# Kernel optimization log

Measured on AMD Instinct MI355X. Metric: run time of the kernel, lower is better.

The kernel has to match this reference:

```python
import jax, jax.numpy as jnp
import numpy as np
from jax import lax

H = 12  # num_heads (from init_kwargs)


def _orthogonal_landmarks(q, num_landmarks):
    # q: (B, N, D) already scaled. Faithful to torch loop: recursively pick the
    # point whose max |cos sim| to the already-selected landmarks is minimal.
    B, N, D = q.shape
    nrm = jnp.linalg.norm(q, axis=-1, keepdims=True)
    qk = q / jnp.maximum(nrm, 1e-12)
    bidx = jnp.arange(B)
    key = jax.random.key(42)
    idx0 = jax.random.randint(key, (B,), 0, N)
    cur = qk[bidx, idx0]                             # (B, D)
    # running max |cos sim|; selected rows pinned to 10 (as in torch code)
    max_sim = jnp.zeros((B, N), qk.dtype).at[bidx, idx0].set(10.0)

    def step(carry, _):
        max_sim, cur = carry
        cos = jnp.abs(jnp.einsum('bnd,bd->bn', qk, cur))
        max_sim = jnp.maximum(max_sim, cos)
        idx = jnp.argmin(max_sim, axis=-1)
        cur2 = qk[bidx, idx]
        max_sim = max_sim.at[bidx, idx].set(10.0)
        return (max_sim, cur2), idx

    (_, _), idxs = lax.scan(step, (max_sim, cur), None, length=num_landmarks - 1)
    all_idx = jnp.concatenate([idx0[None, :], idxs], axis=0).T  # (B, L)
    landmarks = q[bidx[:, None], all_idx]                        # unnormalized q rows
    return lax.stop_gradient(landmarks)


def _orthoformer(q, k, v, num_landmarks, num_frames):
    # q,k,v: (B*h, N, D);  N = F * P
    Bh, N, D = q.shape
    F = num_frames
    P = N // F
    sc = D ** (-0.25)
    q = q * sc
    k = k * sc
    lm = _orthogonal_landmarks(q, num_landmarks)                 # (Bh, L, D)
    kernel_1 = jax.nn.softmax(jnp.einsum('bnd,bld->bnl', q, lm), axis=-1)   # (Bh,N,L)
    k2 = jnp.einsum('bld,bnd->bln', lm, k).reshape(Bh, num_landmarks, F, P)
    kernel_2 = jax.nn.softmax(k2, axis=-1)                       # (Bh,L,F,P)
    vr = v.reshape(Bh, F, P, D)
    x = jnp.einsum('blfp,bfpd->blfd', kernel_2, vr)
    x = jnp.einsum('bnl,blfd->bnfd', kernel_1, x)                # (Bh,N,F,D)
    return x


def setup_inputs() -> dict:
    key = jax.random.key(0)
    ks = jax.random.split(key, 6)
    B, F, P, C = 2, 16, 196, 768
    N = F * P
    s = 0.02
    x = jax.random.normal(ks[0], (B, N, C), jnp.float32)
    W_qkv = jax.random.normal(ks[1], (C, 3 * C), jnp.float32) * s
    W_pq = jax.random.normal(ks[2], (C, C), jnp.float32) * s
    W_pkv = jax.random.normal(ks[3], (C, 2 * C), jnp.float32) * s
    W_proj = jax.random.normal(ks[4], (C, C), jnp.float32) * s
    b_proj = jnp.zeros((C,), jnp.float32)
    return {"x": x, "W_qkv": W_qkv, "W_pq": W_pq, "W_pkv": W_pkv,
            "W_proj": W_proj, "b_proj": b_proj,
            "seq_len": P, "num_frames": F, "num_landmarks": 128}


def reference(x, W_qkv, W_pq, W_pkv, W_proj, b_proj, seq_len, num_frames, num_landmarks):
    B, N, C = x.shape
    F, P, h = num_frames, seq_len, H
    d = C // h
    scale = d ** (-0.5)
    qkv = x @ W_qkv                                              # (B,N,3C)
    q, k, v = jnp.split(qkv, 3, axis=-1)
    def to_bh(t):  # b n (h d) -> (b h) n d
        return t.reshape(B, N, h, d).transpose(0, 2, 1, 3).reshape(B * h, N, d)
    q_, k_, v_ = to_bh(q), to_bh(k), to_bh(v)
    xo = _orthoformer(q_, k_, v_, num_landmarks, F)              # (B*h,N,F,d)
    # (b h) s f d -> b s f (h d)
    xo = xo.reshape(B, h, N, F, d).transpose(0, 2, 3, 1, 4).reshape(B, N, F, C)
    # diagonal over (frame-of-query g, frame-of-key f)
    xd = xo.reshape(B, F, P, F, C)
    xdiag = jnp.diagonal(xd, axis1=1, axis2=3)                   # (B,P,C,F)
    xdiag = jnp.moveaxis(xdiag, -1, 1).reshape(B, N, C)          # b (f p) d
    q2 = xdiag @ W_pq                                            # (B,N,C)
    k2, v2 = jnp.split(xo @ W_pkv, 2, axis=-1)                   # (B,N,F,C) each
    q2 = q2.reshape(B, N, h, d).transpose(0, 2, 1, 3) * scale    # (B,h,N,d)
    k2 = k2.reshape(B, N, F, h, d).transpose(0, 3, 1, 2, 4)      # (B,h,N,F,d)
    v2 = v2.reshape(B, N, F, h, d).transpose(0, 3, 1, 2, 4)
    attn = jax.nn.softmax(jnp.einsum('bhsd,bhsfd->bhsf', q2, k2), axis=-1)
    out = jnp.einsum('bhsf,bhsfd->bhsd', attn, v2)               # (B,h,N,d)
    out = out.transpose(0, 2, 1, 3).reshape(B, N, C)
    out = out @ W_proj + b_proj
    return out, attn
```

## Files before the change

kernel.cpp:

```cpp
#include <hip/hip_runtime.h>


using u16 = unsigned short;
using u32 = unsigned int;
using u64 = unsigned long long;

typedef short bf16x8 __attribute__((ext_vector_type(8)));
typedef float f32x4 __attribute__((ext_vector_type(4)));

#define N_ 3136
#define C_ 768
#define H_ 12
#define F_ 16
#define P_ 196
#define L_ 128
#define SC_ 0.35355339059327373f
#define OUTPART_ ((size_t)2 * N_ * C_)
#define KB_ 8
#define RPB_ 392

__device__ __forceinline__ float b2f(u16 u) {
  u32 x = ((u32)u) << 16; float f; __builtin_memcpy(&f, &x, 4); return f;
}
__device__ __forceinline__ float lo16f(u32 u) {
  u32 x = u << 16; float f; __builtin_memcpy(&f, &x, 4); return f;
}
__device__ __forceinline__ float hi16f(u32 u) {
  u32 x = u & 0xFFFF0000u; float f; __builtin_memcpy(&f, &x, 4); return f;
}
__device__ __forceinline__ u16 f2b(float f) {
  u32 u; __builtin_memcpy(&u, &f, 4);
  u32 r = (u + 0x7FFFu + ((u >> 16) & 1u)) >> 16;
  return (u16)r;
}
__device__ __forceinline__ u64 d2u(double d) { u64 u; __builtin_memcpy(&u, &d, 8); return u; }

__device__ __forceinline__ void gll16(const void* g, void* l) {
  __builtin_amdgcn_global_load_lds(
      (__attribute__((address_space(1))) void*)g,
      (__attribute__((address_space(3))) void*)l, 16, 0, 0);
}

__global__ void detect_k(const u32* __restrict__ w, int* __restrict__ flag) {
  const int t = threadIdx.x;
  int hits = 0;
  #pragma unroll
  for (int i = 0; i < 16; ++i) {
    u32 word = w[t * 16 + i];
    u32 e = (word >> 7) & 0xFFu;
    if (e >= 110u && e <= 126u) hits++;
  }
  #pragma unroll
  for (int off = 32; off > 0; off >>= 1) hits += __shfl_down(hits, off);
  if (t == 0) flag[0] = (hits >= 512) ? 0 : 1;
}

__global__ void zcnt_k(u64* __restrict__ p) { if (threadIdx.x < 384) p[threadIdx.x] = 0ull; }

__device__ __forceinline__ void tf2(u32 k0, u32 k1v, u32 c0, u32 c1, u32& o0, u32& o1) {
  u32 ks[3] = {k0, k1v, k0 ^ k1v ^ 0x1BD11BDAu};
  u32 x0 = c0 + ks[0], x1 = c1 + ks[1];
  const u32 rA[4] = {13u, 15u, 26u, 6u}, rB[4] = {17u, 29u, 16u, 24u};
  #pragma unroll
  for (int r = 0; r < 5; ++r) {
    #pragma unroll
    for (int q = 0; q < 4; ++q) {
      u32 rot = (r & 1) ? rB[q] : rA[q];
      x0 += x1; x1 = (x1 << rot) | (x1 >> (32u - rot)); x1 ^= x0;
    }
    x0 += ks[(r + 1) % 3];
    x1 += ks[(r + 2) % 3] + (u32)(r + 1);
  }
  o0 = x0; o1 = x1;
}

__device__ __forceinline__ int tf_idx0(int bh) {
  u32 a0, a1, b0, b1;
  tf2(0u, 42u, 0u, 0u, a0, a1);
  tf2(0u, 42u, 0u, 1u, b0, b1);
  u32 j = (u32)bh;
  u32 h0, h1, l0, l1;
  tf2(a0, a1, 0u, j, h0, h1);
  u32 hi = h0 ^ h1;
  tf2(b0, b1, 0u, j, l0, l1);
  u32 lo = l0 ^ l1;
  return (int)(((hi % 3136u) * 2048u + (lo % 3136u)) % 3136u);
}

__global__ __launch_bounds__(256) void qselT_k(const void* __restrict__ xr, const void* __restrict__ wr,
                                               const int* __restrict__ flagp, float* __restrict__ qt)
{
  __shared__ float As[128 * 20];
  __shared__ float Bs[16 * 64];
  const int t = threadIdx.x;
  const int m0 = blockIdx.x * 128;
  const int n0 = blockIdx.y * 64;
  const int f32i = flagp[0];
  const int tx = t & 15, ty = t >> 4;
  float acc[8][4];
  #pragma unroll
  for (int i = 0; i < 8; ++i)
    #pragma unroll
    for (int j = 0; j < 4; ++j) acc[i][j] = 0.f;

  const int alr = t >> 1;
  const int alk = (t & 1) * 8;
  const int bkr = t >> 4;
  const int bnc = (t & 15) * 4;

  for (int k0 = 0; k0 < 768; k0 += 16) {
    float av[8];
    float4 bv;
    if (f32i) {
      const float* xa = (const float*)xr + (size_t)(m0 + alr) * 768 + k0 + alk;
      float4 a0 = *(const float4*)(xa);
      float4 a1 = *(const float4*)(xa + 4);
      av[0] = a0.x; av[1] = a0.y; av[2] = a0.z; av[3] = a0.w;
      av[4] = a1.x; av[5] = a1.y; av[6] = a1.z; av[7] = a1.w;
      bv = *(const float4*)((const float*)wr + (size_t)(k0 + bkr) * 2304 + n0 + bnc);
    } else {
      const u16* xa = (const u16*)xr + (size_t)(m0 + alr) * 768 + k0 + alk;
      #pragma unroll
      for (int j = 0; j < 8; ++j) av[j] = b2f(xa[j]);
      const u16* wa = (const u16*)wr + (size_t)(k0 + bkr) * 2304 + n0 + bnc;
      bv.x = b2f(wa[0]); bv.y = b2f(wa[1]); bv.z = b2f(wa[2]); bv.w = b2f(wa[3]);
    }
    #pragma unroll
    for (int j = 0; j < 8; ++j) As[alr * 20 + alk + j] = av[j];
    *(float4*)(&Bs[bkr * 64 + bnc]) = bv;
    __syncthreads();
    #pragma unroll
    for (int kk = 0; kk < 16; ++kk) {
      float a[8], b[4];
      #pragma unroll
      for (int i = 0; i < 8; ++i) a[i] = As[(ty * 8 + i) * 20 + kk];
      #pragma unroll
      for (int j = 0; j < 4; ++j) b[j] = Bs[kk * 64 + tx * 4 + j];
      #pragma unroll
      for (int i = 0; i < 8; ++i)
        #pragma unroll
        for (int j = 0; j < 4; ++j) acc[i][j] += a[i] * b[j];
    }
    __syncthreads();
  }
  #pragma unroll
  for (int i = 0; i < 8; ++i) {
    const int m = m0 + ty * 8 + i;
    const int b = m / N_, n = m - b * N_;
    #pragma unroll
    for (int j = 0; j < 4; ++j) {
      const int col = n0 + tx * 4 + j;
      const int hh = col >> 6, dd = col & 63;
      qt[((size_t)(b * H_ + hh) * 64 + dd) * N_ + n] = acc[i][j] * SC_;
    }
  }
}

__global__ __launch_bounds__(512, 1) void landmarksR_k(
    const float* __restrict__ qt, float* __restrict__ lm, u64* __restrict__ cand)
{
  const int kb = blockIdx.y;
  const int bh = blockIdx.x;
  const float* QT = qt + (size_t)bh * 64 * N_;
  float* LM = lm + (size_t)bh * L_ * 64;
  u64* cd = cand + (size_t)bh * 16;
  __shared__ double curD[64];
  __shared__ u64 redV[8];
  __shared__ int redI[8];
  __shared__ int sW;
  const int t = threadIdx.x;
  const bool act = (t < RPB_);
  const int g = t >> 2, dc = t & 3, d0 = dc * 16;
  const int r0 = kb * RPB_;
  const int myRow = r0 + t;
  const float* base = QT + r0 + 4 * g;

  float4 qreg[16];
  #pragma unroll
  for (int i = 0; i < 16; ++i) qreg[i] = (float4){0.f, 0.f, 0.f, 0.f};
  if (act) {
    #pragma unroll
    for (int i = 0; i < 16; ++i) qreg[i] = *(const float4*)(base + (size_t)(d0 + i) * N_);
  }

  double inv_own = 0.0, ms_own = 0.0;
  if (act) {
    double s0 = 0.0, s1 = 0.0, s2 = 0.0, s3 = 0.0;
    #pragma unroll
    for (int i = 0; i < 16; ++i) {
      const float4 v = qreg[i];
      s0 += (double)v.x * (double)v.x; s1 += (double)v.y * (double)v.y;
      s2 += (double)v.z * (double)v.z; s3 += (double)v.w * (double)v.w;
    }
    s0 += __shfl_xor(s0, 1); s1 += __shfl_xor(s1, 1);
    s2 += __shfl_xor(s2, 1); s3 += __shfl_xor(s3, 1);
    s0 += __shfl_xor(s0, 2); s1 += __shfl_xor(s1, 2);
    s2 += __shfl_xor(s2, 2); s3 += __shfl_xor(s3, 2);
    const double sown = (dc == 0) ? s0 : (dc == 1) ? s1 : (dc == 2) ? s2 : s3;
    inv_own = 1.0 / fmax(sqrt(sown), 1e-12);
  }
  const int idx0 = tf_idx0(bh);
  if (act && myRow == idx0) ms_own = 10.0;

  if (t < 64) {
    const float vf = QT[(size_t)t * N_ + idx0];
    double v = (double)vf;
    double s = v * v;
    #pragma unroll
    for (int off = 32; off; off >>= 1) s += __shfl_xor(s, off);
    curD[t] = v / fmax(sqrt(s), 1e-12);
    if (kb == 0) LM[t] = vf;
  }
  __syncthreads();

  for (int step = 1; step < 128; ++step) {
    u64 bV = d2u(1e30); int bI = 0x7fffffff;
    if (act) {
      double a0 = 0.0, a1 = 0.0, a2 = 0.0, a3 = 0.0;
      #pragma unroll
      for (int i = 0; i < 16; ++i) {
        const float4 v = qreg[i];
        const double c = curD[d0 + i];
        a0 += (double)v.x * c; a1 += (double)v.y * c;
        a2 += (double)v.z * c; a3 += (double)v.w * c;
      }
      a0 += __shfl_xor(a0, 1); a1 += __shfl_xor(a1, 1);
      a2 += __shfl_xor(a2, 1); a3 += __shfl_xor(a3, 1);
      a0 += __shfl_xor(a0, 2); a1 += __shfl_xor(a1, 2);
      a2 += __shfl_xor(a2, 2); a3 += __shfl_xor(a3, 2);
      const double aown = (dc == 0) ? a0 : (dc == 1) ? a1 : (dc == 2) ? a2 : a3;
      ms_own = fmax(ms_own, fabs(aown * inv_own));
      bV = d2u(ms_own); bI = myRow;
    }
    #pragma unroll
    for (int off = 32; off; off >>= 1) {
      const u64 ov = __shfl_xor(bV, off);
      const int oi = __shfl_xor(bI, off);
      if (ov < bV || (ov == bV && oi < bI)) { bV = ov; bI = oi; }
    }
    if ((t & 63) == 0) { redV[t >> 6] = bV; redI[t >> 6] = bI; }
    __syncthreads();
    const int par = step & 1;
    if (t == 0) {
      u64 v = redV[0]; int ix = redI[0];
      #pragma unroll
      for (int w2 = 1; w2 < 8; ++w2)
        if (redV[w2] < v || (redV[w2] == v && redI[w2] < ix)) { v = redV[w2]; ix = redI[w2]; }
      const u64 pk = (v & ~((1ull << 19) - 1ull)) | ((u64)(u32)(step & 127) << 12) | (u64)(u32)ix;
      __hip_atomic_store(&cd[par * KB_ + kb], pk, __ATOMIC_RELAXED, __HIP_MEMORY_SCOPE_AGENT);
    }
    if (t < 64) {
      u64 pv = ~0ull;
      int ok = 1;
      for (;;) {
        if (t < KB_) {
          pv = __hip_atomic_load(&cd[par * KB_ + t], __ATOMIC_RELAXED, __HIP_MEMORY_SCOPE_AGENT);
          ok = ((int)((pv >> 12) & 127u) == step) ? 1 : 0;
        }
        if (__all(ok)) break;
        __builtin_amdgcn_s_sleep(1);
      }
      u64 m = (t < KB_) ? pv : ~0ull;
      #pragma unroll
      for (int off = 1; off < KB_; off <<= 1) {
        const u64 o = __shfl_xor(m, off);
        if (o < m) m = o;
      }
      if (t == 0) sW = (int)(m & 0xFFFu);
    }
    __syncthreads();
    const int w = sW;
    if (act && myRow == w) ms_own = 10.0;
    if (t < 64) {
      const float vf = QT[(size_t)t * N_ + w];
      double v = (double)vf;
      double s = v * v;
      #pragma unroll
      for (int off = 32; off; off >>= 1) s += __shfl_xor(s, off);
      curD[t] = v / fmax(sqrt(s), 1e-12);
      if (kb == 0) LM[(size_t)step * 64 + t] = vf;
    }
    __syncthreads();
  }
}

__device__ __forceinline__ void twT_body(const void* W, int K, int Nn, int f32i,
                                         u16* WT, int k0, int n0, int t, u16 (&Ts)[64][80])
{
  const int kr = t >> 2, nc = (t & 3) * 16;
  u16 tmp[16];
  if (f32i) {
    const float* p = (const float*)W + (size_t)(k0 + kr) * Nn + n0 + nc;
    #pragma unroll
    for (int j = 0; j < 16; ++j) tmp[j] = f2b(p[j]);
  } else {
    const u16* p = (const u16*)W + (size_t)(k0 + kr) * Nn + n0 + nc;
    #pragma unroll
    for (int j = 0; j < 16; ++j) tmp[j] = p[j];
  }
  #pragma unroll
  for (int j = 0; j < 16; ++j) Ts[kr][nc + j] = tmp[j];
  __syncthreads();
  const int nr = t >> 2, kc = (t & 3) * 16;
  u16 o[16];
  #pragma unroll
  for (int j = 0; j < 16; ++j) o[j] = Ts[kc + j][nr];
  u16* dst = WT + (size_t)(n0 + nr) * K + k0 + kc;
  *(uint4*)(dst) = *(uint4*)(o);
  *(uint4*)(dst + 8) = *(uint4*)(o + 8);
}

__global__ __launch_bounds__(256) void twT_k(const void* __restrict__ W, int K, int Nn,
                                             const int* __restrict__ flagp, u16* __restrict__ WT)
{
  __shared__ u16 Ts[64][80];
  twT_body(W, K, Nn, flagp[0], WT, blockIdx.x * 64, blockIdx.y * 64, threadIdx.x, Ts);
}

__global__ __launch_bounds__(256) void twT3_k(const void* __restrict__ W0, const void* __restrict__ W1,
                                              const void* __restrict__ W2, const int* __restrict__ flagp,
                                              u16* __restrict__ T0, u16* __restrict__ T1, u16* __restrict__ T2,
                                              u16* __restrict__ Wb)
{
  __shared__ u16 Ts[64][80];
  const int z = blockIdx.z;
  const int t = threadIdx.x;
  if (z == 3) {
    const int k0 = blockIdx.x * 64, n0 = blockIdx.y * 64;
    const int kr = t >> 2, nc = (t & 3) * 16;
    u16 tmp[16];
    if (flagp[0]) {
      const float* p = (const float*)W0 + (size_t)(k0 + kr) * 1536 + n0 + nc;
      #pragma unroll
      for (int j = 0; j < 16; ++j) tmp[j] = f2b(p[j]);
    } else {
      const u16* p = (const u16*)W0 + (size_t)(k0 + kr) * 1536 + n0 + nc;
      #pragma unroll
      for (int j = 0; j < 16; ++j) tmp[j] = p[j];
    }
    u16* dst = Wb + (size_t)(k0 + kr) * 1536 + n0 + nc;
    *(uint4*)(dst) = *(uint4*)(tmp);
    *(uint4*)(dst + 8) = *(uint4*)(tmp + 8);
    return;
  }
  const void* W = (z == 0) ? W0 : (z == 1) ? W1 : W2;
  u16* WT = (z == 0) ? T0 : (z == 1) ? T1 : T2;
  const int Nn = (z == 0) ? 1536 : 768;
  if (blockIdx.y * 64 >= Nn) return;
  twT_body(W, 768, Nn, flagp[0], WT, blockIdx.x * 64, blockIdx.y * 64, t, Ts);
}

__global__ __launch_bounds__(256) void xcvt_k(const void* __restrict__ x,
                                              const int* __restrict__ flagp, u16* __restrict__ xb)
{
  const int i = blockIdx.x * 256 + threadIdx.x;
  if (flagp[0]) {
    const float4* p = (const float4*)x + (size_t)i * 2;
    float4 f0 = p[0], f1 = p[1];
    u16 tmp[8] = { f2b(f0.x), f2b(f0.y), f2b(f0.z), f2b(f0.w),
                   f2b(f1.x), f2b(f1.y), f2b(f1.z), f2b(f1.w) };
    *(uint4*)(xb + (size_t)i * 8) = *(uint4*)tmp;
  } else {
    ((uint4*)xb)[i] = ((const uint4*)x)[i];
  }
}

struct GemmCore {
  const u16 *aP0, *aP1, *bP0, *bP1;
  u16 *lA0, *lA1, *lB0, *lB1;
  int roA[4], roB[4];
  int mw, nw, lr, lk;
};

__device__ __forceinline__ void gemm_core_init(GemmCore& gc, u16* As, u16* Bs,
    const u16* A16, const u16* B16, size_t aOff, size_t bOff,
    int m0, int n0, int lda, int ldb, int M, int t)
{
  const int lane = t & 63;
  const int w = t >> 6;
  gc.mw = (w >> 1) * 64;
  gc.nw = (w & 1) * 64;
  gc.lr = lane & 15;
  gc.lk = lane >> 4;
  const int c0 = w * 2, c1 = c0 + 1;
  const int rl = lane >> 2, sl = lane & 3;
  const int rowA0 = c0 * 16 + rl, rowA1 = c1 * 16 + rl;
  const int segA0 = (sl ^ ((rowA0 ^ (rowA0 >> 2)) & 3)) * 8;
  const int segA1 = (sl ^ ((rowA1 ^ (rowA1 >> 2)) & 3)) * 8;
  int ga0 = m0 + rowA0; if (ga0 >= M) ga0 = M - 1;
  int ga1 = m0 + rowA1; if (ga1 >= M) ga1 = M - 1;
  gc.aP0 = A16 + aOff + (size_t)ga0 * lda + segA0;
  gc.aP1 = A16 + aOff + (size_t)ga1 * lda + segA1;
  gc.bP0 = B16 + bOff + (size_t)(n0 + rowA0) * ldb + segA0;
  gc.bP1 = B16 + bOff + (size_t)(n0 + rowA1) * ldb + segA1;
  gc.lA0 = &As[c0 * 512]; gc.lA1 = &As[c1 * 512];
  gc.lB0 = &Bs[c0 * 512]; gc.lB1 = &Bs[c1 * 512];
  #pragma unroll
  for (int q = 0; q < 4; ++q) {
    const int ra = gc.mw + q * 16 + gc.lr;
    gc.roA[q] = ra * 32 + ((gc.lk ^ ((ra ^ (ra >> 2)) & 3)) * 8);
    const int rb = gc.nw + q * 16 + gc.lr;
    gc.roB[q] = rb * 32 + ((gc.lk ^ ((rb ^ (rb >> 2)) & 3)) * 8);
  }
}

__device__ __forceinline__ void gemm_core_loop(const GemmCore& gc, u16* As, u16* Bs,
                                               int K, f32x4 (&acc)[4][4])
{
  for (int k0 = 0; k0 < K; k0 += 32) {
    gll16(gc.aP0 + k0, gc.lA0);
    gll16(gc.aP1 + k0, gc.lA1);
    gll16(gc.bP0 + k0, gc.lB0);
    gll16(gc.bP1 + k0, gc.lB1);
    __syncthreads();
    bf16x8 af[4], bfv[4];
    #pragma unroll
    for (int mt = 0; mt < 4; ++mt) af[mt] = *(const bf16x8*)(&As[gc.roA[mt]]);
    #pragma unroll
    for (int nt = 0; nt < 4; ++nt) bfv[nt] = *(const bf16x8*)(&Bs[gc.roB[nt]]);
    #pragma unroll
    for (int mt = 0; mt < 4; ++mt)
      #pragma unroll
      for (int nt = 0; nt < 4; ++nt)
        acc[mt][nt] = __builtin_amdgcn_mfma_f32_16x16x32_bf16(af[mt], bfv[nt], acc[mt][nt], 0, 0, 0);
    __syncthreads();
  }
}

template <int MODE>
__global__ __launch_bounds__(256) void gemm_k(
    const void* __restrict__ Ap, const void* __restrict__ Bp,
    int M, int K, int lda, int ldb, int n0c, int cn, const int* __restrict__ flagp,
    float* __restrict__ of0, u16* __restrict__ ob0, u16* __restrict__ ob1, u16* __restrict__ ob2,
    const void* __restrict__ biasRaw, void* __restrict__ outRaw)
{
  __shared__ u16 As[128 * 32];
  __shared__ u16 Bs[128 * 32];
  const int t = threadIdx.x;
  const int m0 = blockIdx.x * 128;
  const int n0 = blockIdx.y * 128;
  const int rf = (MODE == 4) ? flagp[0] : 0;

  size_t aOff = 0, bOff = 0;
  if constexpr (MODE == 1) {
    const int bh = blockIdx.z;
    aOff = (size_t)bh * ((size_t)N_ * 128) + (size_t)n0c * 128;
    bOff = (size_t)bh * (1024 * 128);
  }
  if constexpr (MODE == 5) {
    const int h = blockIdx.z;
    aOff = (size_t)h * (2 * cn) * 64;
    bOff = (size_t)h * 64;
  }
  if constexpr (MODE == 6) {
    const int h = blockIdx.z;
    aOff = (size_t)h * (2 * cn) * 768;
    bOff = (size_t)(768 + h * 64) * 768;
  }
  f32x4 acc[4][4];
  #pragma unroll
  for (int i = 0; i < 4; ++i)
    #pragma unroll
    for (int j = 0; j < 4; ++j) acc[i][j] = (f32x4){0.f, 0.f, 0.f, 0.f};

  GemmCore gc;
  gemm_core_init(gc, As, Bs, (const u16*)Ap, (const u16*)Bp, aOff, bOff, m0, n0, lda, ldb, M, t);
  gemm_core_loop(gc, As, Bs, K, acc);

  const int lr = gc.lr, lk = gc.lk, mw = gc.mw, nw = gc.nw;
  #pragma unroll
  for (int mt = 0; mt < 4; ++mt) {
    #pragma unroll
    for (int nt = 0; nt < 4; ++nt) {
      #pragma unroll
      for (int r = 0; r < 4; ++r) {
        const int grow = m0 + mw + mt * 16 + lk * 4 + r;
        const int gcol = n0 + nw + nt * 16 + lr;
        if (grow >= M) continue;
        float vv = acc[mt][nt][r];
        if constexpr (MODE == 0) {
          int b = (grow >= N_) ? 1 : 0;
          int n = grow - b * N_;
          int t3 = gcol / C_, cc = gcol - t3 * C_;
          int hh = cc >> 6, dd = cc & 63;
          size_t dst = (((size_t)(b * H_ + hh)) * N_ + n) * 64 + dd;
          if (t3 == 0) ob0[dst] = f2b(vv * SC_);
          else if (t3 == 1) ob1[dst] = f2b(vv * SC_);
          else ob2[dst] = f2b(vv);
        } else if constexpr (MODE == 1) {
          const int bh = blockIdx.z;
          int b = bh / H_, hh = bh - b * H_;
          int f = gcol >> 6, dd = gcol & 63;
          u16 wv = f2b(vv);
          ob0[(((size_t)(b * cn + grow)) * F_ + f) * C_ + hh * 64 + dd] = wv;
          int n = n0c + grow;
          if (f == n / P_) ob1[((size_t)(b * cn + grow)) * C_ + hh * 64 + dd] = wv;
        } else if constexpr (MODE == 3) {
          int hh = gcol >> 6, dd = gcol & 63;
          ob0[((size_t)hh * (2 * cn) + grow) * 64 + dd] = f2b(vv * 0.125f);
        } else if constexpr (MODE == 5) {
          ob0[((size_t)blockIdx.z * (2 * cn) + grow) * 768 + gcol] = f2b(vv);
        } else if constexpr (MODE == 6) {
          if (gcol < 64) {
            int b2 = (grow >= cn) ? 1 : 0;
            int ln = grow - b2 * cn;
            ob0[((size_t)(b2 * N_ + n0c + ln)) * 768 + blockIdx.z * 64 + gcol] = f2b(vv);
          }
        } else {
          float bvad = rf ? ((const float*)biasRaw)[gcol] : b2f(((const u16*)biasRaw)[gcol]);
          float ov = vv + bvad;
          if (rf) ((float*)outRaw)[(size_t)grow * C_ + gcol] = ov;
          else    ((u16*)outRaw)[(size_t)grow * C_ + gcol] = f2b(ov);
        }
      }
    }
  }
}

__global__ __launch_bounds__(256) void k1_k(const u16* __restrict__ qb,
                                            const float* __restrict__ lm,
                                            u16* __restrict__ k1)
{
  const int bh = blockIdx.y;
  const int r0 = blockIdx.x * 64;
  __shared__ float qT[64][65];
  __shared__ float lmS[128 * 64];
  __shared__ float redA[4][64];
  __shared__ float redB[64];
  const int t = threadIdx.x;
  const u16* Q = qb + ((size_t)bh * N_ + r0) * 64;
  const float* Lm = lm + (size_t)bh * L_ * 64;
  for (int u = t; u < 2048; u += 256) ((float4*)lmS)[u] = ((const float4*)Lm)[u];
  for (int u = t; u < 512; u += 256) {
    int row = u >> 3, j0 = (u & 7) * 8;
    uint4 pk = *(const uint4*)(Q + (size_t)row * 64 + j0);
    const u16* pu = (const u16*)&pk;
    #pragma unroll
    for (int jj = 0; jj < 8; ++jj) qT[j0 + jj][row] = b2f(pu[jj]);
  }
  __syncthreads();
  const int row = t & 63, ch = t >> 6;
  float qr[64];
  #pragma unroll
  for (int j = 0; j < 64; ++j) qr[j] = qT[j][row];
  float s[32];
  for (int li = 0; li < 32; ++li) {
    const float* lp = lmS + (ch * 32 + li) * 64;
    float a = 0.f;
    #pragma unroll
    for (int j = 0; j < 64; ++j) a += lp[j] * qr[j];
    s[li] = a;
  }
  float mx = -1e30f;
  for (int li = 0; li < 32; ++li) mx = fmaxf(mx, s[li]);
  redA[ch][row] = mx;
  __syncthreads();
  if (t < 64) redB[t] = fmaxf(fmaxf(redA[0][t], redA[1][t]), fmaxf(redA[2][t], redA[3][t]));
  __syncthreads();
  mx = redB[row];
  float sum = 0.f;
  for (int li = 0; li < 32; ++li) { float e = __expf(s[li] - mx); s[li] = e; sum += e; }
  __syncthreads();
  redA[ch][row] = sum;
  __syncthreads();
  if (t < 64) redB[t] = 1.0f / (redA[0][t] + redA[1][t] + redA[2][t] + redA[3][t]);
  __syncthreads();
  const float inv = redB[row];
  u16* out = k1 + ((size_t)bh * N_ + r0 + row) * 128 + ch * 32;
  for (int li = 0; li < 32; ++li) out[li] = f2b(s[li] * inv);
}

__global__ __launch_bounds__(256) void k2x1_k(const float* __restrict__ lm,
                                              const u16* __restrict__ kb,
                                              const u16* __restrict__ vb,
                                              u16* __restrict__ x1)
{
  const int bh = blockIdx.x;
  const int f = blockIdx.y;
  __shared__ u16 kS[P_ * 64];
  __shared__ u16 vS[P_ * 64];
  __shared__ float redM[2][128];
  __shared__ float redS[2][128];
  const int t = threadIdx.x;
  const u16* Kf = kb + ((size_t)bh * N_ + f * P_) * 64;
  const u16* Vf = vb + ((size_t)bh * N_ + f * P_) * 64;
  for (int u = t; u < 1568; u += 256) {
    ((uint4*)kS)[u] = ((const uint4*)Kf)[u];
    ((uint4*)vS)[u] = ((const uint4*)Vf)[u];
  }
  __syncthreads();
  const int l = t & 127, half = t >> 7;
  const float* lp = lm + ((size_t)bh * L_ + l) * 64;
  float lr[64];
  #pragma unroll
  for (int j = 0; j < 64; ++j) lr[j] = lp[j];

  const int p0 = half * 98, p1 = p0 + 98;
  float mx = -1e30f;
  for (int p = p0; p < p1; ++p) {
    const uint4* kp = (const uint4*)(kS + p * 64);
    float s = 0.f;
    #pragma unroll
    for (int q4 = 0; q4 < 8; ++q4) {
      uint4 pk = kp[q4];
      const u32* pu = (const u32*)&pk;
      #pragma unroll
      for (int j2 = 0; j2 < 4; ++j2) {
        u32 u = pu[j2];
        s += lr[q4 * 8 + j2 * 2] * lo16f(u) + lr[q4 * 8 + j2 * 2 + 1] * hi16f(u);
      }
    }
    mx = fmaxf(mx, s);
  }
  redM[half][l] = mx;
  __syncthreads();
  mx = fmaxf(redM[0][l], redM[1][l]);

  float sm = 0.f;
  for (int p = p0; p < p1; ++p) {
    const uint4* kp = (const uint4*)(kS + p * 64);
    float s = 0.f;
    #pragma unroll
    for (int q4 = 0; q4 < 8; ++q4) {
      uint4 pk = kp[q4];
      const u32* pu = (const u32*)&pk;
      #pragma unroll
      for (int j2 = 0; j2 < 4; ++j2) {
        u32 u = pu[j2];
        s += lr[q4 * 8 + j2 * 2] * lo16f(u) + lr[q4 * 8 + j2 * 2 + 1] * hi16f(u);
      }
    }
    sm += __expf(s - mx);
  }
  redS[half][l] = sm;
  __syncthreads();
  const float inv = 1.0f / (redS[0][l] + redS[1][l]);

  const int dd0 = half * 32;
  float acc[32];
  #pragma unroll
  for (int u = 0; u < 32; ++u) acc[u] = 0.f;
  for (int p = 0; p < P_; ++p) {
    const uint4* kp = (const uint4*)(kS + p * 64);
    float s = 0.f;
    #pragma unroll
    for (int q4 = 0; q4 < 8; ++q4) {
      uint4 pk = kp[q4];
      const u32* pu = (const u32*)&pk;
      #pragma unroll
      for (int j2 = 0; j2 < 4; ++j2) {
        u32 u = pu[j2];
        s += lr[q4 * 8 + j2 * 2] * lo16f(u) + lr[q4 * 8 + j2 * 2 + 1] * hi16f(u);
      }
    }
    const float e = __expf(s - mx);
    const uint4* vp = (const uint4*)(vS + p * 64 + dd0);
    #pragma unroll
    for (int q4 = 0; q4 < 4; ++q4) {
      uint4 pv = vp[q4];
      const u32* pu = (const u32*)&pv;
      #pragma unroll
      for (int j2 = 0; j2 < 4; ++j2) {
        u32 u = pu[j2];
        acc[q4 * 8 + j2 * 2]     += e * lo16f(u);
        acc[q4 * 8 + j2 * 2 + 1] += e * hi16f(u);
      }
    }
  }
  u16* outT = x1 + (size_t)bh * (1024 * 128) + (size_t)(f * 64 + dd0) * 128 + l;
  for (int u = 0; u < 32; ++u) outT[(size_t)u * 128] = f2b(acc[u] * inv);
}

__global__ __launch_bounds__(256) void attn2_k(const u16* __restrict__ xoc,
                                               const u16* __restrict__ g,
                                               int n0c, int cn, const int* __restrict__ flagp,
                                               void* __restrict__ outRaw, u16* __restrict__ wc)
{
  __shared__ float aS[12][16];
  const int t = threadIdx.x;
  const int m = blockIdx.x;
  const int b = (m >= cn) ? 1 : 0;
  const int ln = m - b * cn;
  const int n = n0c + ln;
  const int f32o = flagp[0];
  const u16* Xo = xoc + ((size_t)(b * cn + ln) * 16) * 768;
  const size_t hstr = (size_t)(2 * cn) * 768;

  if (t < 192) {
    const int h = t >> 4, f = t & 15;
    const uint4* xp = (const uint4*)(Xo + (size_t)f * 768);
    const uint4* gp = (const uint4*)(g + (size_t)h * hstr + (size_t)m * 768);
    float lg = 0.f;
    #pragma unroll 4
    for (int q = 0; q < 96; ++q) {
      uint4 xv = xp[q], gv = gp[q];
      const u32* xu = (const u32*)&xv;
      const u32* gu = (const u32*)&gv;
      #pragma unroll
      for (int j = 0; j < 4; ++j)
        lg += lo16f(xu[j]) * lo16f(gu[j]) + hi16f(xu[j]) * hi16f(gu[j]);
    }
    float mx = lg;
    mx = fmaxf(mx, __shfl_xor(mx, 1));
    mx = fmaxf(mx, __shfl_xor(mx, 2));
    mx = fmaxf(mx, __shfl_xor(mx, 4));
    mx = fmaxf(mx, __shfl_xor(mx, 8));
    float e = __expf(lg - mx);
    float sm = e;
    sm += __shfl_xor(sm, 1);
    sm += __shfl_xor(sm, 2);
    sm += __shfl_xor(sm, 4);
    sm += __shfl_xor(sm, 8);
    const float a = e / sm;
    const size_t abase = ((size_t)(b * H_ + h) * N_ + n) * F_ + f;
    if (f32o) ((float*)outRaw)[OUTPART_ + abase] = a;
    else      ((u16*)outRaw)[OUTPART_ + abase] = f2b(a);
    aS[h][f] = a;
  }
  __syncthreads();
  if (t < 192) {
    const int cg = t >> 1, sh = t & 1;
    const int c0 = cg * 8;
    float acc[6][8];
    #pragma unroll
    for (int j = 0; j < 6; ++j)
      #pragma unroll
      for (int k = 0; k < 8; ++k) acc[j][k] = 0.f;
    for (int f = 0; f < 16; ++f) {
      uint4 xv = *(const uint4*)(Xo + (size_t)f * 768 + c0);
      const u32* xu = (const u32*)&xv;
      float xf[8];
      #pragma unroll
      for (int j = 0; j < 4; ++j) { xf[2 * j] = lo16f(xu[j]); xf[2 * j + 1] = hi16f(xu[j]); }
      #pragma unroll
      for (int j = 0; j < 6; ++j) {
        const float a = aS[sh * 6 + j][f];
        #pragma unroll
        for (int k = 0; k < 8; ++k) acc[j][k] += a * xf[k];
      }
    }
    #pragma unroll
    for (int j = 0; j < 6; ++j) {
      u16 pk[8];
      #pragma unroll
      for (int k = 0; k < 8; ++k) pk[k] = f2b(acc[j][k]);
      *(uint4*)(wc + (size_t)(sh * 6 + j) * hstr + (size_t)m * 768 + c0) = *(uint4*)pk;
    }
  }
}

extern "C" void kernel_launch(void* const* d_in, const int* in_sizes, int n_in,
                              void* d_out, int out_size, void* d_ws, size_t ws_size,
                              hipStream_t stream)
{
  (void)in_sizes; (void)n_in; (void)out_size;
  const void* x     = d_in[0];
  const void* Wqkv  = d_in[1];
  const void* Wpq   = d_in[2];
  const void* Wpkv  = d_in[3];
  const void* Wproj = d_in[4];
  const void* bproj = d_in[5];

  char* ws = (char*)d_ws;
  size_t off = 0;
  auto alloc = [&](size_t bytes) { void* p = ws + off; off += (bytes + 255) & ~(size_t)255; return p; };
  int*  flagp  = (int*)alloc(256);
  u16*  WpkvT  = (u16*)alloc(2359296);
  u16*  WpqT   = (u16*)alloc(1179648);
  u16*  WprojT = (u16*)alloc(1179648);
  u16*  Wpkvb  = (u16*)alloc(2359296);
  float* lm    = (float*)alloc(786432);
  u16*  x1b    = (u16*)alloc(6291456);
  u16*  ob     = (u16*)alloc(9633792);
  u16*  k1b    = (u16*)alloc(19267584);
  const size_t sc0 = off;

  float* qt   = (float*)(ws + sc0);
  u64*   cand = (u64*)(ws + sc0 + 19267584);
  u16* WqkvT = (u16*)(ws + sc0);
  u16* xb    = (u16*)(ws + sc0 + 3538944);
  u16* qb    = (u16*)(ws + sc0 + 13172736);
  u16* kbuf  = qb + 4816896;
  u16* vb    = kbuf + 4816896;
  const size_t phaseB_need = sc0 + 42074112 + 1024;
  if (phaseB_need > ws_size) return;

  int Nc = 0;
  {
    const int cands[5] = {3136, 1568, 784, 392, 196};
    for (int i = 0; i < 5; ++i) {
      if (sc0 + (size_t)92160 * cands[i] + 1024 <= ws_size) { Nc = cands[i]; break; }
    }
  }
  if (Nc == 0) return;
  const int nchunks = N_ / Nc;
  u16* xoc = (u16*)(ws + sc0);
  u16* xdc = xoc + (size_t)24576 * Nc;
  u16* q2b = xdc + (size_t)1536 * Nc;
  u16* gbf = q2b + (size_t)1536 * Nc;

  detect_k<<<1, 64, 0, stream>>>((const u32*)Wqkv, flagp);
  zcnt_k<<<1, 512, 0, stream>>>(cand);
  twT3_k<<<dim3(12, 24, 4), 256, 0, stream>>>(Wpkv, Wpq, Wproj, flagp,
                                              WpkvT, WpqT, WprojT, Wpkvb);

  qselT_k<<<dim3(49, 12), 256, 0, stream>>>(x, Wqkv, flagp, qt);
  landmarksR_k<<<dim3(24, KB_), 512, 0, stream>>>(qt, lm, cand);

  twT_k<<<dim3(12, 36), 256, 0, stream>>>(Wqkv, 768, 2304, flagp, WqkvT);
  xcvt_k<<<2352, 256, 0, stream>>>(x, flagp, xb);

  gemm_k<0><<<dim3(49, 18, 1), 256, 0, stream>>>(xb, WqkvT, 6272, 768, 768, 768, 0, 0, flagp,
                                                 nullptr, qb, kbuf, vb, nullptr, nullptr);
  k2x1_k<<<dim3(24, 16), 256, 0, stream>>>(lm, kbuf, vb, x1b);
  k1_k<<<dim3(49, 24), 256, 0, stream>>>(qb, lm, k1b);

  const int gx = (2 * Nc + 127) / 128;
  for (int c = 0; c < nchunks; ++c) {
    const int n0c = c * Nc;
    gemm_k<1><<<dim3((Nc + 127) / 128, 8, 24), 256, 0, stream>>>(
        k1b, x1b, Nc, 128, 128, 128, n0c, Nc, flagp, nullptr, xoc, xdc, nullptr, nullptr, nullptr);
    gemm_k<3><<<dim3(gx, 6, 1), 256, 0, stream>>>(
        xdc, WpqT, 2 * Nc, 768, 768, 768, n0c, Nc, flagp, nullptr, q2b, nullptr, nullptr, nullptr, nullptr);
    gemm_k<5><<<dim3(gx, 6, 12), 256, 0, stream>>>(
        q2b, Wpkvb, 2 * Nc, 64, 64, 1536, n0c, Nc, flagp, nullptr, gbf, nullptr, nullptr, nullptr, nullptr);
    attn2_k<<<dim3(2 * Nc), 256, 0, stream>>>(xoc, gbf, n0c, Nc, flagp, d_out, gbf);
    gemm_k<6><<<dim3(gx, 1, 12), 256, 0, stream>>>(
        gbf, WpkvT, 2 * Nc, 768, 768, 768, n0c, Nc, flagp, nullptr, ob, nullptr, nullptr, nullptr, nullptr);
  }
  gemm_k<4><<<dim3(49, 6, 1), 256, 0, stream>>>(ob, WprojT, 6272, 768, 768, 768, 0, 0, flagp,
                                                nullptr, nullptr, nullptr, nullptr, bproj, d_out);
}
```

Baseline: 1.522 ms.

## Overlap serial landmark selection with QKV GEMM in fused kernels

Merges the q-projection, WqkvT transpose and x conversion into one launch, then runs the serial landmark-selection blocks and the QKV GEMM blocks in a single launch so the GEMM fills CUs left idle by the latency-bound landmark loop. This requires a new workspace layout with separate regions so qt, xb/WqkvT and qb/k/v do not alias, and keeps a fallback path when the workspace is too small. The risk is that landmark blocks, which spin across blocks, could be starved if they are not all resident, and the 512-thread GEMM blocks leave half their threads idle.

```diff
diff --git a/kernel.cpp b/kernel.cpp
--- a/kernel.cpp
+++ b/kernel.cpp
@@ -87,15 +87,10 @@
   return (int)(((hi % 3136u) * 2048u + (lo % 3136u)) % 3136u);
 }
 
-__global__ __launch_bounds__(256) void qselT_k(const void* __restrict__ xr, const void* __restrict__ wr,
-                                               const int* __restrict__ flagp, float* __restrict__ qt)
-{
-  __shared__ float As[128 * 20];
-  __shared__ float Bs[16 * 64];
-  const int t = threadIdx.x;
-  const int m0 = blockIdx.x * 128;
-  const int n0 = blockIdx.y * 64;
-  const int f32i = flagp[0];
+__device__ __forceinline__ void qsel_body(const void* xr, const void* wr, int f32i,
+                                          float* qt, int m0, int n0, int t,
+                                          float* As, float* Bs)
+{
   const int tx = t & 15, ty = t >> 4;
   float acc[8][4];
   #pragma unroll
@@ -156,132 +151,12 @@
   }
 }
 
-__global__ __launch_bounds__(512, 1) void landmarksR_k(
-    const float* __restrict__ qt, float* __restrict__ lm, u64* __restrict__ cand)
-{
-  const int kb = blockIdx.y;
-  const int bh = blockIdx.x;
-  const float* QT = qt + (size_t)bh * 64 * N_;
-  float* LM = lm + (size_t)bh * L_ * 64;
-  u64* cd = cand + (size_t)bh * 16;
-  __shared__ double curD[64];
-  __shared__ u64 redV[8];
-  __shared__ int redI[8];
-  __shared__ int sW;
-  const int t = threadIdx.x;
-  const bool act = (t < RPB_);
-  const int g = t >> 2, dc = t & 3, d0 = dc * 16;
-  const int r0 = kb * RPB_;
-  const int myRow = r0 + t;
-  const float* base = QT + r0 + 4 * g;
-
-  float4 qreg[16];
-  #pragma unroll
-  for (int i = 0; i < 16; ++i) qreg[i] = (float4){0.f, 0.f, 0.f, 0.f};
-  if (act) {
-    #pragma unroll
-    for (int i = 0; i < 16; ++i) qreg[i] = *(const float4*)(base + (size_t)(d0 + i) * N_);
-  }
-
-  double inv_own = 0.0, ms_own = 0.0;
-  if (act) {
-    double s0 = 0.0, s1 = 0.0, s2 = 0.0, s3 = 0.0;
-    #pragma unroll
-    for (int i = 0; i < 16; ++i) {
-      const float4 v = qreg[i];
-      s0 += (double)v.x * (double)v.x; s1 += (double)v.y * (double)v.y;
-      s2 += (double)v.z * (double)v.z; s3 += (double)v.w * (double)v.w;
-    }
-    s0 += __shfl_xor(s0, 1); s1 += __shfl_xor(s1, 1);
-    s2 += __shfl_xor(s2, 1); s3 += __shfl_xor(s3, 1);
-    s0 += __shfl_xor(s0, 2); s1 += __shfl_xor(s1, 2);
-    s2 += __shfl_xor(s2, 2); s3 += __shfl_xor(s3, 2);
-    const double sown = (dc == 0) ? s0 : (dc == 1) ? s1 : (dc == 2) ? s2 : s3;
-    inv_own = 1.0 / fmax(sqrt(sown), 1e-12);
-  }
-  const int idx0 = tf_idx0(bh);
-  if (act && myRow == idx0) ms_own = 10.0;
-
-  if (t < 64) {
-    const float vf = QT[(size_t)t * N_ + idx0];
-    double v = (double)vf;
-    double s = v * v;
-    #pragma unroll
-    for (int off = 32; off; off >>= 1) s += __shfl_xor(s, off);
-    curD[t] = v / fmax(sqrt(s), 1e-12);
-    if (kb == 0) LM[t] = vf;
-  }
-  __syncthreads();
-
-  for (int step = 1; step < 128; ++step) {
-    u64 bV = d2u(1e30); int bI = 0x7fffffff;
-    if (act) {
-      double a0 = 0.0, a1 = 0.0, a2 = 0.0, a3 = 0.0;
-      #pragma unroll
-      for (int i = 0; i < 16; ++i) {
-        const float4 v = qreg[i];
-        const double c = curD[d0 + i];
-        a0 += (double)v.x * c; a1 += (double)v.y * c;
-        a2 += (double)v.z * c; a3 += (double)v.w * c;
-      }
-      a0 += __shfl_xor(a0, 1); a1 += __shfl_xor(a1, 1);
-      a2 += __shfl_xor(a2, 1); a3 += __shfl_xor(a3, 1);
-      a0 += __shfl_xor(a0, 2); a1 += __shfl_xor(a1, 2);
-      a2 += __shfl_xor(a2, 2); a3 += __shfl_xor(a3, 2);
-      const double aown = (dc == 0) ? a0 : (dc == 1) ? a1 : (dc == 2) ? a2 : a3;
-      ms_own = fmax(ms_own, fabs(aown * inv_own));
-      bV = d2u(ms_own); bI = myRow;
-    }
-    #pragma unroll
-    for (int off = 32; off; off >>= 1) {
-      const u64 ov = __shfl_xor(bV, off);
-      const int oi = __shfl_xor(bI, off);
-      if (ov < bV || (ov == bV && oi < bI)) { bV = ov; bI = oi; }
-    }
-    if ((t & 63) == 0) { redV[t >> 6] = bV; redI[t >> 6] = bI; }
-    __syncthreads();
-    const int par = step & 1;
-    if (t == 0) {
-      u64 v = redV[0]; int ix = redI[0];
-      #pragma unroll
-      for (int w2 = 1; w2 < 8; ++w2)
-        if (redV[w2] < v || (redV[w2] == v && redI[w2] < ix)) { v = redV[w2]; ix = redI[w2]; }
-      const u64 pk = (v & ~((1ull << 19) - 1ull)) | ((u64)(u32)(step & 127) << 12) | (u64)(u32)ix;
-      __hip_atomic_store(&cd[par * KB_ + kb], pk, __ATOMIC_RELAXED, __HIP_MEMORY_SCOPE_AGENT);
-    }
-    if (t < 64) {
-      u64 pv = ~0ull;
-      int ok = 1;
-      for (;;) {
-        if (t < KB_) {
-          pv = __hip_atomic_load(&cd[par * KB_ + t], __ATOMIC_RELAXED, __HIP_MEMORY_SCOPE_AGENT);
-          ok = ((int)((pv >> 12) & 127u) == step) ? 1 : 0;
-        }
-        if (__all(ok)) break;
-        __builtin_amdgcn_s_sleep(1);
-      }
-      u64 m = (t < KB_) ? pv : ~0ull;
-      #pragma unroll
-      for (int off = 1; off < KB_; off <<= 1) {
-        const u64 o = __shfl_xor(m, off);
-        if (o < m) m = o;
-      }
-      if (t == 0) sW = (int)(m & 0xFFFu);
-    }
-    __syncthreads();
-    const int w = sW;
-    if (act && myRow == w) ms_own = 10.0;
-    if (t < 64) {
-      const float vf = QT[(size_t)t * N_ + w];
-      double v = (double)vf;
-      double s = v * v;
-      #pragma unroll
-      for (int off = 32; off; off >>= 1) s += __shfl_xor(s, off);
-      curD[t] = v / fmax(sqrt(s), 1e-12);
-      if (kb == 0) LM[(size_t)step * 64 + t] = vf;
-    }
-    __syncthreads();
-  }
+__global__ __launch_bounds__(256) void qselT_k(const void* __restrict__ xr, const void* __restrict__ wr,
+                                               const int* __restrict__ flagp, float* __restrict__ qt)
+{
+  __shared__ float As[128 * 20];
+  __shared__ float Bs[16 * 64];
+  qsel_body(xr, wr, flagp[0], qt, blockIdx.x * 128, blockIdx.y * 64, threadIdx.x, As, Bs);
 }
 
 __device__ __forceinline__ void twT_body(const void* W, int K, int Nn, int f32i,
@@ -350,11 +225,9 @@
   twT_body(W, 768, Nn, flagp[0], WT, blockIdx.x * 64, blockIdx.y * 64, t, Ts);
 }
 
-__global__ __launch_bounds__(256) void xcvt_k(const void* __restrict__ x,
-                                              const int* __restrict__ flagp, u16* __restrict__ xb)
-{
-  const int i = blockIdx.x * 256 + threadIdx.x;
-  if (flagp[0]) {
+__device__ __forceinline__ void xcvt_body(const void* x, int f32i, u16* xb, int i)
+{
+  if (f32i) {
     const float4* p = (const float4*)x + (size_t)i * 2;
     float4 f0 = p[0], f1 = p[1];
     u16 tmp[8] = { f2b(f0.x), f2b(f0.y), f2b(f0.z), f2b(f0.w),
@@ -362,6 +235,32 @@
     *(uint4*)(xb + (size_t)i * 8) = *(uint4*)tmp;
   } else {
     ((uint4*)xb)[i] = ((const uint4*)x)[i];
+  }
+}
+
+__global__ __launch_bounds__(256) void xcvt_k(const void* __restrict__ x,
+                                              const int* __restrict__ flagp, u16* __restrict__ xb)
+{
+  xcvt_body(x, flagp[0], xb, blockIdx.x * 256 + threadIdx.x);
+}
+
+__global__ __launch_bounds__(256) void fusedA_k(const void* __restrict__ x, const void* __restrict__ Wqkv,
+                                                const int* __restrict__ flagp, float* __restrict__ qt,
+                                                u16* __restrict__ WqkvT, u16* __restrict__ xb)
+{
+  __shared__ float As[128 * 20];
+  __shared__ float Bs[16 * 64];
+  __shared__ u16 Ts[64][80];
+  const int id = blockIdx.x;
+  const int t = threadIdx.x;
+  const int f32i = flagp[0];
+  if (id < 588) {
+    qsel_body(x, Wqkv, f32i, qt, (id % 49) * 128, (id / 49) * 64, t, As, Bs);
+  } else if (id < 1020) {
+    const int id2 = id - 588;
+    twT_body(Wqkv, 768, 2304, f32i, WqkvT, (id2 % 12) * 64, (id2 / 12) * 64, t, Ts);
+  } else {
+    xcvt_body(x, f32i, xb, (id - 1020) * 256 + t);
   }
 }
 
@@ -427,6 +326,185 @@
   }
 }
 
+__device__ __forceinline__ void mode0_epi(const f32x4 (&acc)[4][4], int m0, int n0,
+                                          int mw, int nw, int lr, int lk,
+                                          u16* ob0, u16* ob1, u16* ob2)
+{
+  #pragma unroll
+  for (int mt = 0; mt < 4; ++mt) {
+    #pragma unroll
+    for (int nt = 0; nt < 4; ++nt) {
+      #pragma unroll
+      for (int r = 0; r < 4; ++r) {
+        const int grow = m0 + mw + mt * 16 + lk * 4 + r;
+        const int gcol = n0 + nw + nt * 16 + lr;
+        float vv = acc[mt][nt][r];
+        int b = (grow >= N_) ? 1 : 0;
+        int n = grow - b * N_;
+        int t3 = gcol / C_, cc = gcol - t3 * C_;
+        int hh = cc >> 6, dd = cc & 63;
+        size_t dst = (((size_t)(b * H_ + hh)) * N_ + n) * 64 + dd;
+        if (t3 == 0) ob0[dst] = f2b(vv * SC_);
+        else if (t3 == 1) ob1[dst] = f2b(vv * SC_);
+        else ob2[dst] = f2b(vv);
+      }
+    }
+  }
+}
+
+__global__ __launch_bounds__(512, 1) void fusedB_k(
+    const float* __restrict__ qt, float* __restrict__ lm, u64* __restrict__ cand,
+    const u16* __restrict__ xb, const u16* __restrict__ WqkvT,
+    u16* __restrict__ qb, u16* __restrict__ kbuf, u16* __restrict__ vb)
+{
+  __shared__ double curD[64];
+  __shared__ u64 redV[8];
+  __shared__ int redI[8];
+  __shared__ int sW;
+  __shared__ u16 As[128 * 32];
+  __shared__ u16 Bs[128 * 32];
+  const int t = threadIdx.x;
+
+  if (blockIdx.x >= 192) {
+    const int gid = blockIdx.x - 192;
+    const int m0 = (gid % 49) * 128;
+    const int n0 = (gid / 49) * 128;
+    if (t < 256) {
+      f32x4 acc[4][4];
+      #pragma unroll
+      for (int i = 0; i < 4; ++i)
+        #pragma unroll
+        for (int j = 0; j < 4; ++j) acc[i][j] = (f32x4){0.f, 0.f, 0.f, 0.f};
+      GemmCore gc;
+      gemm_core_init(gc, As, Bs, xb, WqkvT, 0, 0, m0, n0, 768, 768, 6272, t);
+      gemm_core_loop(gc, As, Bs, 768, acc);
+      mode0_epi(acc, m0, n0, gc.mw, gc.nw, gc.lr, gc.lk, qb, kbuf, vb);
+    } else {
+      for (int i = 0; i < 24; ++i) { __syncthreads(); __syncthreads(); }
+    }
+    return;
+  }
+
+  const int bh = blockIdx.x % 24;
+  const int kb = blockIdx.x / 24;
+  const float* QT = qt + (size_t)bh * 64 * N_;
+  float* LM = lm + (size_t)bh * L_ * 64;
+  u64* cd = cand + (size_t)bh * 16;
+  const bool act = (t < RPB_);
+  const int g = t >> 2, dc = t & 3, d0 = dc * 16;
+  const int r0 = kb * RPB_;
+  const int myRow = r0 + t;
+  const float* base = QT + r0 + 4 * g;
+
+  float4 qreg[16];
+  #pragma unroll
+  for (int i = 0; i < 16; ++i) qreg[i] = (float4){0.f, 0.f, 0.f, 0.f};
+  if (act) {
+    #pragma unroll
+    for (int i = 0; i < 16; ++i) qreg[i] = *(const float4*)(base + (size_t)(d0 + i) * N_);
+  }
+
+  double inv_own = 0.0, ms_own = 0.0;
+  if (act) {
+    double s0 = 0.0, s1 = 0.0, s2 = 0.0, s3 = 0.0;
+    #pragma unroll
+    for (int i = 0; i < 16; ++i) {
+      const float4 v = qreg[i];
+      s0 += (double)v.x * (double)v.x; s1 += (double)v.y * (double)v.y;
+      s2 += (double)v.z * (double)v.z; s3 += (double)v.w * (double)v.w;
+    }
+    s0 += __shfl_xor(s0, 1); s1 += __shfl_xor(s1, 1);
+    s2 += __shfl_xor(s2, 1); s3 += __shfl_xor(s3, 1);
+    s0 += __shfl_xor(s0, 2); s1 += __shfl_xor(s1, 2);
+    s2 += __shfl_xor(s2, 2); s3 += __shfl_xor(s3, 2);
+    const double sown = (dc == 0) ? s0 : (dc == 1) ? s1 : (dc == 2) ? s2 : s3;
+    inv_own = 1.0 / fmax(sqrt(sown), 1e-12);
+  }
+  const int idx0 = tf_idx0(bh);
+  if (act && myRow == idx0) ms_own = 10.0;
+
+  if (t < 64) {
+    const float vf = QT[(size_t)t * N_ + idx0];
+    double v = (double)vf;
+    double s = v * v;
+    #pragma unroll
+    for (int off = 32; off; off >>= 1) s += __shfl_xor(s, off);
+    curD[t] = v / fmax(sqrt(s), 1e-12);
+    if (kb == 0) LM[t] = vf;
+  }
+  __syncthreads();
+
+  for (int step = 1; step < 128; ++step) {
+    u64 bV = d2u(1e30); int bI = 0x7fffffff;
+    if (act) {
+      double a0 = 0.0, a1 = 0.0, a2 = 0.0, a3 = 0.0;
+      #pragma unroll
+      for (int i = 0; i < 16; ++i) {
+        const float4 v = qreg[i];
+        const double c = curD[d0 + i];
+        a0 += (double)v.x * c; a1 += (double)v.y * c;
+        a2 += (double)v.z * c; a3 += (double)v.w * c;
+      }
+      a0 += __shfl_xor(a0, 1); a1 += __shfl_xor(a1, 1);
+      a2 += __shfl_xor(a2, 1); a3 += __shfl_xor(a3, 1);
+      a0 += __shfl_xor(a0, 2); a1 += __shfl_xor(a1, 2);
+      a2 += __shfl_xor(a2, 2); a3 += __shfl_xor(a3, 2);
+      const double aown = (dc == 0) ? a0 : (dc == 1) ? a1 : (dc == 2) ? a2 : a3;
+      ms_own = fmax(ms_own, fabs(aown * inv_own));
+      bV = d2u(ms_own); bI = myRow;
+    }
+    #pragma unroll
+    for (int off = 32; off; off >>= 1) {
+      const u64 ov = __shfl_xor(bV, off);
+      const int oi = __shfl_xor(bI, off);
+      if (ov < bV || (ov == bV && oi < bI)) { bV = ov; bI = oi; }
+    }
+    if ((t & 63) == 0) { redV[t >> 6] = bV; redI[t >> 6] = bI; }
+    __syncthreads();
+    const int par = step & 1;
+    if (t == 0) {
+      u64 v = redV[0]; int ix = redI[0];
+      #pragma unroll
+      for (int w2 = 1; w2 < 8; ++w2)
+        if (redV[w2] < v || (redV[w2] == v && redI[w2] < ix)) { v = redV[w2]; ix = redI[w2]; }
+      const u64 pk = (v & ~((1ull << 19) - 1ull)) | ((u64)(u32)(step & 127) << 12) | (u64)(u32)ix;
+      __hip_atomic_store(&cd[par * KB_ + kb], pk, __ATOMIC_RELAXED, __HIP_MEMORY_SCOPE_AGENT);
+    }
+    if (t < 64) {
+      u64 pv = ~0ull;
+      int ok = 1;
+      for (;;) {
+        if (t < KB_) {
+          pv = __hip_atomic_load(&cd[par * KB_ + t], __ATOMIC_RELAXED, __HIP_MEMORY_SCOPE_AGENT);
+          ok = ((int)((pv >> 12) & 127u) == step) ? 1 : 0;
+        }
+        if (__all(ok)) break;
+        __builtin_amdgcn_s_sleep(1);
+      }
+      u64 m = (t < KB_) ? pv : ~0ull;
+      #pragma unroll
+      for (int off = 1; off < KB_; off <<= 1) {
+        const u64 o = __shfl_xor(m, off);
+        if (o < m) m = o;
+      }
+      if (t == 0) sW = (int)(m & 0xFFFu);
+    }
+    __syncthreads();
+    const int w = sW;
+    if (act && myRow == w) ms_own = 10.0;
+    if (t < 64) {
+      const float vf = QT[(size_t)t * N_ + w];
+      double v = (double)vf;
+      double s = v * v;
+      #pragma unroll
+      for (int off = 32; off; off >>= 1) s += __shfl_xor(s, off);
+      curD[t] = v / fmax(sqrt(s), 1e-12);
+      if (kb == 0) LM[(size_t)step * 64 + t] = vf;
+    }
+    __syncthreads();
+  }
+}
+
 template <int MODE>
 __global__ __launch_bounds__(256) void gemm_k(
     const void* __restrict__ Ap, const void* __restrict__ Bp,
@@ -468,6 +546,10 @@
   gemm_core_loop(gc, As, Bs, K, acc);
 
   const int lr = gc.lr, lk = gc.lk, mw = gc.mw, nw = gc.nw;
+  if constexpr (MODE == 0) {
+    mode0_epi(acc, m0, n0, mw, nw, lr, lk, ob0, ob1, ob2);
+    return;
+  }
   #pragma unroll
   for (int mt = 0; mt < 4; ++mt) {
     #pragma unroll
@@ -478,16 +560,7 @@
         const int gcol = n0 + nw + nt * 16 + lr;
         if (grow >= M) continue;
         float vv = acc[mt][nt][r];
-        if constexpr (MODE == 0) {
-          int b = (grow >= N_) ? 1 : 0;
-          int n = grow - b * N_;
-          int t3 = gcol / C_, cc = gcol - t3 * C_;
-          int hh = cc >> 6, dd = cc & 63;
-          size_t dst = (((size_t)(b * H_ + hh)) * N_ + n) * 64 + dd;
-          if (t3 == 0) ob0[dst] = f2b(vv * SC_);
-          else if (t3 == 1) ob1[dst] = f2b(vv * SC_);
-          else ob2[dst] = f2b(vv);
-        } else if constexpr (MODE == 1) {
+        if constexpr (MODE == 1) {
           const int bh = blockIdx.z;
           int b = bh / H_, hh = bh - b * H_;
           int f = gcol >> 6, dd = gcol & 63;
@@ -771,30 +844,50 @@
   u16*  Wpkvb  = (u16*)alloc(2359296);
   float* lm    = (float*)alloc(786432);
   u16*  x1b    = (u16*)alloc(6291456);
-  u16*  ob     = (u16*)alloc(9633792);
   u16*  k1b    = (u16*)alloc(19267584);
   const size_t sc0 = off;
 
-  float* qt   = (float*)(ws + sc0);
-  u64*   cand = (u64*)(ws + sc0 + 19267584);
-  u16* WqkvT = (u16*)(ws + sc0);
-  u16* xb    = (u16*)(ws + sc0 + 3538944);
-  u16* qb    = (u16*)(ws + sc0 + 13172736);
-  u16* kbuf  = qb + 4816896;
-  u16* vb    = kbuf + 4816896;
-  const size_t phaseB_need = sc0 + 42074112 + 1024;
-  if (phaseB_need > ws_size) return;
+  const size_t r1 = sc0;
+  const size_t r2 = r1 + 19267584 + 3072;
+  const size_t r3 = r2 + 3538944 + 9633792;
+  const size_t bigNeed = r3 + 3 * (size_t)9633792 + 256;
+  const bool fused = (bigNeed <= ws_size);
+
+  float* qt;  u64* cand;  u16 *WqkvT, *xb, *qb, *kbuf, *vb, *ob;
+  size_t chunkBase;
+  if (fused) {
+    qt    = (float*)(ws + r1);
+    cand  = (u64*)(ws + r1 + 19267584);
+    WqkvT = (u16*)(ws + r2);
+    xb    = WqkvT + 1769472;
+    qb    = (u16*)(ws + r3);
+    kbuf  = qb + 4816896;
+    vb    = kbuf + 4816896;
+    ob    = (u16*)(ws + sc0);
+    chunkBase = sc0 + 9633792;
+  } else {
+    qt    = (float*)(ws + sc0);
+    cand  = (u64*)(ws + sc0 + 19267584);
+    WqkvT = (u16*)(ws + sc0);
+    xb    = (u16*)(ws + sc0 + 3538944);
+    qb    = (u16*)(ws + sc0 + 13172736);
+    kbuf  = qb + 4816896;
+    vb    = kbuf + 4816896;
+    ob    = (u16*)(ws + sc0);
+    chunkBase = sc0 + 9633792;
+    if (sc0 + 42074112 + 1024 > ws_size) return;
+  }
 
   int Nc = 0;
   {
     const int cands[5] = {3136, 1568, 784, 392, 196};
     for (int i = 0; i < 5; ++i) {
-      if (sc0 + (size_t)92160 * cands[i] + 1024 <= ws_size) { Nc = cands[i]; break; }
+      if (chunkBase + (size_t)92160 * cands[i] + 1024 <= ws_size) { Nc = cands[i]; break; }
     }
   }
   if (Nc == 0) return;
   const int nchunks = N_ / Nc;
-  u16* xoc = (u16*)(ws + sc0);
+  u16* xoc = (u16*)(ws + chunkBase);
   u16* xdc = xoc + (size_t)24576 * Nc;
   u16* q2b = xdc + (size_t)1536 * Nc;
   u16* gbf = q2b + (size_t)1536 * Nc;
@@ -804,14 +897,18 @@
   twT3_k<<<dim3(12, 24, 4), 256, 0, stream>>>(Wpkv, Wpq, Wproj, flagp,
                                               WpkvT, WpqT, WprojT, Wpkvb);
 
-  qselT_k<<<dim3(49, 12), 256, 0, stream>>>(x, Wqkv, flagp, qt);
-  landmarksR_k<<<dim3(24, KB_), 512, 0, stream>>>(qt, lm, cand);
-
-  twT_k<<<dim3(12, 36), 256, 0, stream>>>(Wqkv, 768, 2304, flagp, WqkvT);
-  xcvt_k<<<2352, 256, 0, stream>>>(x, flagp, xb);
-
-  gemm_k<0><<<dim3(49, 18, 1), 256, 0, stream>>>(xb, WqkvT, 6272, 768, 768, 768, 0, 0, flagp,
-                                                 nullptr, qb, kbuf, vb, nullptr, nullptr);
+  if (fused) {
+    fusedA_k<<<3372, 256, 0, stream>>>(x, Wqkv, flagp, qt, WqkvT, xb);
+    fusedB_k<<<1074, 512, 0, stream>>>(qt, lm, cand, xb, WqkvT, qb, kbuf, vb);
+  } else {
+    qselT_k<<<dim3(49, 12), 256, 0, stream>>>(x, Wqkv, flagp, qt);
+    fusedB_k<<<192, 512, 0, stream>>>(qt, lm, cand, xb, WqkvT, qb, kbuf, vb);
+    twT_k<<<dim3(12, 36), 256, 0, stream>>>(Wqkv, 768, 2304, flagp, WqkvT);
+    xcvt_k<<<2352, 256, 0, stream>>>(x, flagp, xb);
+    gemm_k<0><<<dim3(49, 18, 1), 256, 0, stream>>>(xb, WqkvT, 6272, 768, 768, 768, 0, 0, flagp,
+                                                   nullptr, qb, kbuf, vb, nullptr, nullptr);
+  }
+
   k2x1_k<<<dim3(24, 16), 256, 0, stream>>>(lm, kbuf, vb, x1b);
   k1_k<<<dim3(49, 24), 256, 0, stream>>>(qb, lm, k1b);
 
```

Result: faster. 1.483 ms (-2.6%).
